# Performance work log

Hardware: AMD Instinct MI355X
Metric: run time of the kernel (lower is better)

## Reference

```python
import jax, jax.numpy as jnp
import numpy as np

N_NODES = 100000
N_EDGES = 1600000
DIM_IN, DIM_HID, DIM_OUT = 64, 128, 40


def setup_inputs() -> dict:
    key = jax.random.key(0)
    ks = jax.random.split(key, 6)
    x = jax.random.normal(ks[0], (N_NODES, DIM_IN), dtype=jnp.float32)
    edge_index = jax.random.randint(ks[1], (2, N_EDGES), 0, N_NODES, dtype=jnp.int64)
    s_in = 1.0 / np.sqrt(DIM_IN)
    s_hid = 1.0 / np.sqrt(DIM_HID)
    W1l = jax.random.normal(ks[2], (DIM_HID, DIM_IN), dtype=jnp.float32) * s_in
    W1r = jax.random.normal(ks[3], (DIM_HID, DIM_IN), dtype=jnp.float32) * s_in
    b1 = jnp.zeros((DIM_HID,), dtype=jnp.float32)
    W2l = jax.random.normal(ks[4], (DIM_OUT, DIM_HID), dtype=jnp.float32) * s_hid
    W2r = jax.random.normal(ks[5], (DIM_OUT, DIM_HID), dtype=jnp.float32) * s_hid
    b2 = jnp.zeros((DIM_OUT,), dtype=jnp.float32)
    return {"x": x, "edge_index": edge_index, "W1l": W1l, "b1": b1,
            "W1r": W1r, "W2l": W2l, "b2": b2, "W2r": W2r}


def _sage_conv(h, src, dst, Wl, bl, Wr, n_nodes):
    # mean aggregation of source-node features into target nodes
    msg = h[src]                                      # [E, d]
    agg = jax.ops.segment_sum(msg, dst, num_segments=n_nodes)
    cnt = jax.ops.segment_sum(jnp.ones((src.shape[0],), h.dtype), dst,
                              num_segments=n_nodes)
    agg = agg / jnp.maximum(cnt, 1.0)[:, None]        # [N, d]
    # PyG SAGEConv: lin_l(agg) + bias + lin_r(x) (root weight, no bias)
    return agg @ Wl.T + bl + h @ Wr.T


def reference(x, edge_index, W1l, b1, W1r, W2l, b2, W2r):
    src, dst = edge_index[0], edge_index[1]
    n = x.shape[0]
    h = _sage_conv(x, src, dst, W1l, b1, W1r, n)
    h = jax.nn.relu(h)
    out = _sage_conv(h, src, dst, W2l, b2, W2r, n)
    return jax.nn.log_softmax(out, axis=-1)
```

## Files before the change

kernel.cpp:

```cpp
#include <hip/hip_runtime.h>
#include <math.h>

#define NN 100000
#define DI 64
#define DH 128
#define DO 40

#define NBUCK 512
#define NPB 196
#define CAP 3712
#define CAPP 4352
#define EPB 4096
#define TPB_S 512
#define KE (EPB / TPB_S)

typedef __attribute__((ext_vector_type(8))) short bf16x8;
typedef __attribute__((ext_vector_type(4))) float f32x4;
typedef __attribute__((ext_vector_type(2))) float f32x2;

__device__ __forceinline__ unsigned short bf16r(float a) {
    unsigned u = __float_as_uint(a);
    u = (u + 0x7FFF + ((u >> 16) & 1)) >> 16;
    return (unsigned short)u;
}
__device__ __forceinline__ unsigned bf16pair(float a, float b) {
    return (unsigned)bf16r(a) | ((unsigned)bf16r(b) << 16);
}
__device__ __forceinline__ float bflo(unsigned u) { return __uint_as_float(u << 16); }
__device__ __forceinline__ float bfhi(unsigned u) { return __uint_as_float(u & 0xFFFF0000u); }

__global__ __launch_bounds__(TPB_S) void setup_scatter_kernel(
        const float* __restrict__ x, const float* __restrict__ W1l,
        const float* __restrict__ W1r, const float* __restrict__ W2l,
        const float* __restrict__ W2r,
        unsigned* __restrict__ xb, unsigned short* __restrict__ WB1,
        unsigned short* __restrict__ WB2, unsigned* __restrict__ p2,
        const int* __restrict__ src, const int* __restrict__ dst,
        int* __restrict__ bcur, int* __restrict__ eb,
        int nbe, int E, int N) {
    __shared__ int h[NBUCK];
    int t = threadIdx.x;
    if ((int)blockIdx.x < nbe) {
        if (t < NBUCK) h[t] = 0;
        __syncthreads();
        int base = blockIdx.x * EPB;
        int end = base + EPB; if (end > E) end = E;
        int dloc[KE];
#pragma unroll
        for (int k = 0; k < KE; k++) {
            int i = base + t + k * TPB_S;
            dloc[k] = (i < end) ? dst[i] : -1;
        }
#pragma unroll
        for (int k = 0; k < KE; k++)
            if (dloc[k] >= 0) atomicAdd(&h[(unsigned)dloc[k] / NPB], 1);
        __syncthreads();
        if (t < NBUCK) {
            int v = h[t];
            h[t] = v ? (atomicAdd(&bcur[t], v) + t * CAP) : 0;
        }
        __syncthreads();
#pragma unroll
        for (int k = 0; k < KE; k++) {
            int d = dloc[k];
            if (d >= 0) {
                unsigned bk = (unsigned)d / NPB;
                int local = d - (int)bk * NPB;
                int pos = atomicAdd(&h[bk], 1);
                eb[pos] = (local << 17) | src[base + t + k * TPB_S];
            }
        }
    } else {
        int idx = (blockIdx.x - nbe) * TPB_S + t;
        if (idx < (N + 1) * 32) {
            if (idx < N * 32) {
                float2 f = ((const float2*)x)[idx];
                xb[idx] = bf16pair(f.x, f.y);
            } else {
                xb[idx] = 0;
            }
        }
        if (idx < 16384) {
            int j = idx & 7, lane = (idx >> 3) & 63, ks = (idx >> 9) & 3, nt = idx >> 11;
            int k = ks * 32 + (lane >> 4) * 8 + j;
            int n = nt * 16 + (lane & 15);
            float v = (k < DI) ? W1l[n * DI + k] : W1r[n * DI + (k - DI)];
            WB1[idx] = bf16r(v);
        }
        if (idx >= 16384 && idx < 16384 + 10240) {
            int idx2 = idx - 16384;
            int j = idx2 & 7, lane = (idx2 >> 3) & 63, ks = (idx2 >> 9) & 3, nt = idx2 >> 11;
            int k = ks * 32 + (lane >> 4) * 8 + j;
            int n = nt * 16 + (lane & 15);
            float v = (n < DO) ? W2l[n * DH + k] : W2r[(n - DO) * DH + k];
            WB2[idx2] = bf16r(v);
        }
        if (idx < 10) p2[(size_t)N * 10 + idx] = 0;
    }
}

__global__ __launch_bounds__(256) void bucket_fill_kernel(const int* __restrict__ eb,
                                                          const int* __restrict__ bend,
                                                          int* __restrict__ rowptr,
                                                          int* __restrict__ cntg,
                                                          float* __restrict__ inv,
                                                          int* __restrict__ col, int N) {
    __shared__ int scnt[256];
    __shared__ int scur[256];
    __shared__ int sbase[256];
    int b = blockIdx.x, t = threadIdx.x;
    int ebeg = b * CAP, eend = ebeg + bend[b];
    scnt[t] = 0;
    __syncthreads();
    for (int i = ebeg + t; i < eend; i += 256)
        atomicAdd(&scnt[eb[i] >> 17], 1);
    __syncthreads();
    int myc = scnt[t];
    int pc = (myc + 3) & ~3;
    scnt[t] = pc;
    __syncthreads();
    for (int off = 1; off < 256; off <<= 1) {
        int tmp = (t >= off) ? scnt[t - off] : 0;
        __syncthreads();
        scnt[t] += tmp;
        __syncthreads();
    }
    int excl = scnt[t] - pc;
    int base = b * CAPP + excl;
    int node = b * NPB + t;
    if (t < NPB && node < N) {
        rowptr[node] = base;
        cntg[node] = myc;
        inv[node] = 1.0f / (float)(myc > 0 ? myc : 1);
    }
    scur[t] = base;
    sbase[t] = base;
    __syncthreads();
    for (int i = ebeg + t; i < eend; i += 256) {
        int pk = eb[i];
        int pos = atomicAdd(&scur[pk >> 17], 1);
        col[pos] = pk & 0x1FFFF;
    }
    __syncthreads();
    if (t < NPB) {
        int bs = sbase[t];
        for (int i = myc; i < pc; i++) col[bs + i] = NN;
    }
}

__global__ void agg1_kernel(const unsigned* __restrict__ xb, const int* __restrict__ rowptr,
                            const int* __restrict__ cnt, const float* __restrict__ inv,
                            const int* __restrict__ col, unsigned* __restrict__ xa, int N) {
    int n = (blockIdx.x * 256 + threadIdx.x) >> 3;
    int chunk = threadIdx.x & 7;
    if (n >= N) return;
    int beg = rowptr[n], deg = cnt[n];
    int degp = (deg + 3) & ~3;
    float a[8];
#pragma unroll
    for (int j = 0; j < 8; j++) a[j] = 0.f;
    for (int i = 0; i < degp; i += 4) {
        int s0 = col[beg + i], s1 = col[beg + i + 1];
        int s2 = col[beg + i + 2], s3 = col[beg + i + 3];
        uint4 u0 = *(const uint4*)(xb + (size_t)s0 * 32 + chunk * 4);
        uint4 u1 = *(const uint4*)(xb + (size_t)s1 * 32 + chunk * 4);
        uint4 u2 = *(const uint4*)(xb + (size_t)s2 * 32 + chunk * 4);
        uint4 u3 = *(const uint4*)(xb + (size_t)s3 * 32 + chunk * 4);
        a[0] += bflo(u0.x) + bflo(u1.x) + bflo(u2.x) + bflo(u3.x);
        a[1] += bfhi(u0.x) + bfhi(u1.x) + bfhi(u2.x) + bfhi(u3.x);
        a[2] += bflo(u0.y) + bflo(u1.y) + bflo(u2.y) + bflo(u3.y);
        a[3] += bfhi(u0.y) + bfhi(u1.y) + bfhi(u2.y) + bfhi(u3.y);
        a[4] += bflo(u0.z) + bflo(u1.z) + bflo(u2.z) + bflo(u3.z);
        a[5] += bfhi(u0.z) + bfhi(u1.z) + bfhi(u2.z) + bfhi(u3.z);
        a[6] += bflo(u0.w) + bflo(u1.w) + bflo(u2.w) + bflo(u3.w);
        a[7] += bfhi(u0.w) + bfhi(u1.w) + bfhi(u2.w) + bfhi(u3.w);
    }
    float invn = inv[n];
    uint4 o;
    o.x = bf16pair(a[0] * invn, a[1] * invn);
    o.y = bf16pair(a[2] * invn, a[3] * invn);
    o.z = bf16pair(a[4] * invn, a[5] * invn);
    o.w = bf16pair(a[6] * invn, a[7] * invn);
    *(uint4*)(xa + (size_t)n * 64 + chunk * 4) = o;
    uint4 u = *(const uint4*)(xb + (size_t)n * 32 + chunk * 4);
    *(uint4*)(xa + (size_t)n * 64 + 32 + chunk * 4) = u;
}

__global__ __launch_bounds__(256) void gemm12_kernel(const unsigned short* __restrict__ xa,
                                                     const unsigned short* __restrict__ WB1,
                                                     const float* __restrict__ b1,
                                                     const unsigned short* __restrict__ WB2,
                                                     const float* __restrict__ b2,
                                                     unsigned* __restrict__ p2,
                                                     float* __restrict__ selfp, int N) {
    __shared__ unsigned short hs[64][136];
    __shared__ float st[64][41];
    int w = threadIdx.x >> 6, lane = threadIdx.x & 63;
    int quad = lane >> 4, m = lane & 15;
    int rbase = blockIdx.x * 64 + w * 16;
    int arow = rbase + m; if (arow >= N) arow = N - 1;
    int lw = w * 16;

    f32x4 acc[8];
#pragma unroll
    for (int nt = 0; nt < 8; nt++) acc[nt] = (f32x4)(0.f);
#pragma unroll
    for (int ks = 0; ks < 4; ks++) {
        bf16x8 a = *(const bf16x8*)(xa + (size_t)arow * 128 + ks * 32 + quad * 8);
#pragma unroll
        for (int nt = 0; nt < 8; nt++) {
            bf16x8 b = *(const bf16x8*)(WB1 + ((size_t)(nt * 4 + ks) * 64 + lane) * 8);
            acc[nt] = __builtin_amdgcn_mfma_f32_16x16x32_bf16(a, b, acc[nt], 0, 0, 0);
        }
    }
#pragma unroll
    for (int nt = 0; nt < 8; nt++) {
        int colj = nt * 16 + m;
        float bj = b1[colj];
#pragma unroll
        for (int r = 0; r < 4; r++) {
            hs[lw + quad * 4 + r][colj] = bf16r(fmaxf(acc[nt][r] + bj, 0.f));
        }
    }
    __syncthreads();

    f32x4 acc2[5];
#pragma unroll
    for (int nt = 0; nt < 5; nt++) acc2[nt] = (f32x4)(0.f);
#pragma unroll
    for (int ks = 0; ks < 4; ks++) {
        bf16x8 a = *(const bf16x8*)(&hs[lw + m][ks * 32 + quad * 8]);
#pragma unroll
        for (int nt = 0; nt < 5; nt++) {
            bf16x8 b = *(const bf16x8*)(WB2 + ((size_t)(nt * 4 + ks) * 64 + lane) * 8);
            acc2[nt] = __builtin_amdgcn_mfma_f32_16x16x32_bf16(a, b, acc2[nt], 0, 0, 0);
        }
    }
#pragma unroll
    for (int nt = 0; nt < 5; nt++) {
        int colj = nt * 16 + m;
#pragma unroll
        for (int r = 0; r < 4; r++) {
            int lrow = lw + quad * 4 + r;
            int row = rbase + quad * 4 + r;
            float v = acc2[nt][r];
            if (colj < 40) {
                st[lrow][colj] = v;
            } else if (row < N) {
                selfp[(size_t)row * 40 + (colj - 40)] = v + b2[colj - 40];
            }
        }
    }
    __syncthreads();
    for (int i = threadIdx.x; i < 64 * 10; i += 256) {
        int lr = i / 10, dw = i - lr * 10;
        int grow = blockIdx.x * 64 + lr;
        if (grow < N) {
            float v0 = st[lr][dw * 4 + 0], v1 = st[lr][dw * 4 + 1];
            float v2 = st[lr][dw * 4 + 2], v3 = st[lr][dw * 4 + 3];
            unsigned u = __builtin_amdgcn_cvt_pk_fp8_f32(v0, v1, 0u, false);
            u = __builtin_amdgcn_cvt_pk_fp8_f32(v2, v3, u, true);
            p2[(size_t)grow * 10 + dw] = u;
        }
    }
}

__global__ void agg2_softmax_kernel(const unsigned* __restrict__ p2,
                                    const float* __restrict__ selfp,
                                    const int* __restrict__ rowptr,
                                    const int* __restrict__ cnt,
                                    const float* __restrict__ inv,
                                    const int* __restrict__ col,
                                    float* __restrict__ out, int N) {
    int n = (blockIdx.x * 256 + threadIdx.x) >> 3;
    int chunk = threadIdx.x & 7;
    if (n >= N) return;
    int beg = rowptr[n], deg = cnt[n];
    int degp = (deg + 3) & ~3;
    bool vc = (chunk < 5);
    float a[8];
#pragma unroll
    for (int j = 0; j < 8; j++) a[j] = 0.f;
    for (int i = 0; i < degp; i += 4) {
        int s0 = col[beg + i], s1 = col[beg + i + 1];
        int s2 = col[beg + i + 2], s3 = col[beg + i + 3];
        if (vc) {
            uint2 u0 = *(const uint2*)(p2 + (size_t)s0 * 10 + chunk * 2);
            uint2 u1 = *(const uint2*)(p2 + (size_t)s1 * 10 + chunk * 2);
            uint2 u2 = *(const uint2*)(p2 + (size_t)s2 * 10 + chunk * 2);
            uint2 u3 = *(const uint2*)(p2 + (size_t)s3 * 10 + chunk * 2);
            f32x2 d;
            d = __builtin_amdgcn_cvt_pk_f32_fp8(u0.x, false); a[0] += d.x; a[1] += d.y;
            d = __builtin_amdgcn_cvt_pk_f32_fp8(u0.x, true);  a[2] += d.x; a[3] += d.y;
            d = __builtin_amdgcn_cvt_pk_f32_fp8(u0.y, false); a[4] += d.x; a[5] += d.y;
            d = __builtin_amdgcn_cvt_pk_f32_fp8(u0.y, true);  a[6] += d.x; a[7] += d.y;
            d = __builtin_amdgcn_cvt_pk_f32_fp8(u1.x, false); a[0] += d.x; a[1] += d.y;
            d = __builtin_amdgcn_cvt_pk_f32_fp8(u1.x, true);  a[2] += d.x; a[3] += d.y;
            d = __builtin_amdgcn_cvt_pk_f32_fp8(u1.y, false); a[4] += d.x; a[5] += d.y;
            d = __builtin_amdgcn_cvt_pk_f32_fp8(u1.y, true);  a[6] += d.x; a[7] += d.y;
            d = __builtin_amdgcn_cvt_pk_f32_fp8(u2.x, false); a[0] += d.x; a[1] += d.y;
            d = __builtin_amdgcn_cvt_pk_f32_fp8(u2.x, true);  a[2] += d.x; a[3] += d.y;
            d = __builtin_amdgcn_cvt_pk_f32_fp8(u2.y, false); a[4] += d.x; a[5] += d.y;
            d = __builtin_amdgcn_cvt_pk_f32_fp8(u2.y, true);  a[6] += d.x; a[7] += d.y;
            d = __builtin_amdgcn_cvt_pk_f32_fp8(u3.x, false); a[0] += d.x; a[1] += d.y;
            d = __builtin_amdgcn_cvt_pk_f32_fp8(u3.x, true);  a[2] += d.x; a[3] += d.y;
            d = __builtin_amdgcn_cvt_pk_f32_fp8(u3.y, false); a[4] += d.x; a[5] += d.y;
            d = __builtin_amdgcn_cvt_pk_f32_fp8(u3.y, true);  a[6] += d.x; a[7] += d.y;
        }
    }
    float invn = inv[n];
    float v[8];
    if (vc) {
        float4 s0 = *(const float4*)(selfp + (size_t)n * DO + chunk * 8);
        float4 s1 = *(const float4*)(selfp + (size_t)n * DO + chunk * 8 + 4);
        v[0] = a[0] * invn + s0.x; v[1] = a[1] * invn + s0.y;
        v[2] = a[2] * invn + s0.z; v[3] = a[3] * invn + s0.w;
        v[4] = a[4] * invn + s1.x; v[5] = a[5] * invn + s1.y;
        v[6] = a[6] * invn + s1.z; v[7] = a[7] * invn + s1.w;
    } else {
#pragma unroll
        for (int j = 0; j < 8; j++) v[j] = 0.f;
    }
    float mv = -INFINITY;
    if (vc) {
#pragma unroll
        for (int j = 0; j < 8; j++) mv = fmaxf(mv, v[j]);
    }
#pragma unroll
    for (int off = 1; off <= 4; off <<= 1) mv = fmaxf(mv, __shfl_xor(mv, off, 8));
    float es = 0.f;
    if (vc) {
#pragma unroll
        for (int j = 0; j < 8; j++) es += expf(v[j] - mv);
    }
#pragma unroll
    for (int off = 1; off <= 4; off <<= 1) es += __shfl_xor(es, off, 8);
    if (vc) {
        float ls = mv + logf(es);
        float4 o0, o1;
        o0.x = v[0] - ls; o0.y = v[1] - ls; o0.z = v[2] - ls; o0.w = v[3] - ls;
        o1.x = v[4] - ls; o1.y = v[5] - ls; o1.z = v[6] - ls; o1.w = v[7] - ls;
        *(float4*)(out + (size_t)n * DO + chunk * 8) = o0;
        *(float4*)(out + (size_t)n * DO + chunk * 8 + 4) = o1;
    }
}

extern "C" void kernel_launch(void* const* d_in, const int* in_sizes, int n_in,
                              void* d_out, int out_size, void* d_ws, size_t ws_size,
                              hipStream_t stream) {
    const float* x   = (const float*)d_in[0];
    const int*  ei   = (const int*)d_in[1];
    const float* W1l = (const float*)d_in[2];
    const float* b1  = (const float*)d_in[3];
    const float* W1r = (const float*)d_in[4];
    const float* W2l = (const float*)d_in[5];
    const float* b2  = (const float*)d_in[6];
    const float* W2r = (const float*)d_in[7];
    float* out = (float*)d_out;

    const int E = in_sizes[1] / 2;
    const int N = NN;
    const int* src = ei;
    const int* dst = ei + E;
    const int nbe = (E + EPB - 1) / EPB;
    const int nsetup = ((N + 1) * 32 + TPB_S - 1) / TPB_S;

    size_t off = 0;
    auto alloc = [&](size_t nf) { size_t o = off; off += (nf + 63) & ~(size_t)63; return o; };
    size_t o_bcur   = alloc(NBUCK);
    size_t o_eb     = alloc((size_t)NBUCK * CAP);
    size_t o_col    = alloc((size_t)NBUCK * CAPP);
    size_t o_rowptr = alloc(N);
    size_t o_cnt    = alloc(N);
    size_t o_inv    = alloc(N);
    size_t o_xb     = alloc((size_t)(N + 1) * 32);
    size_t o_xa     = alloc((size_t)N * 64);
    size_t o_p2     = alloc((size_t)(N + 1) * 10);
    size_t o_selfp  = alloc((size_t)N * DO);
    size_t o_wb1    = alloc(16384 / 2);
    size_t o_wb2    = alloc(10240 / 2);
    (void)ws_size;

    float* ws = (float*)d_ws;
    int* bcur   = (int*)(ws + o_bcur);
    int* eb     = (int*)(ws + o_eb);
    int* col    = (int*)(ws + o_col);
    int* rowptr = (int*)(ws + o_rowptr);
    int* cnt    = (int*)(ws + o_cnt);
    float* inv  = ws + o_inv;
    unsigned* xb = (unsigned*)(ws + o_xb);
    unsigned* xa = (unsigned*)(ws + o_xa);
    unsigned* p2 = (unsigned*)(ws + o_p2);
    float* selfp = ws + o_selfp;
    unsigned short* WB1 = (unsigned short*)(ws + o_wb1);
    unsigned short* WB2 = (unsigned short*)(ws + o_wb2);

    hipMemsetAsync(bcur, 0, NBUCK * sizeof(int), stream);

    setup_scatter_kernel<<<nbe + nsetup, TPB_S, 0, stream>>>(
        x, W1l, W1r, W2l, W2r, xb, WB1, WB2, p2, src, dst, bcur, eb, nbe, E, N);

    bucket_fill_kernel<<<NBUCK, 256, 0, stream>>>(eb, bcur, rowptr, cnt, inv, col, N);

    agg1_kernel<<<(N * 8 + 255) / 256, 256, 0, stream>>>(xb, rowptr, cnt, inv, col, xa, N);
    gemm12_kernel<<<(N + 63) / 64, 256, 0, stream>>>((const unsigned short*)xa, WB1, b1,
                                                     WB2, b2, p2, selfp, N);
    agg2_softmax_kernel<<<(N * 8 + 255) / 256, 256, 0, stream>>>(p2, selfp, rowptr, cnt, inv, col, out, N);
}
```

Before: 203.4 us.

## Fuse layer-1 neighbor aggregation into the GEMM kernel via shared memory

The first-layer mean aggregation and the two fused GEMMs now run in one kernel. Each block gathers and averages neighbor features for its 64 nodes into shared memory and then feeds them directly to the MFMA stage. This removes the xa intermediate buffer's global write and read and one kernel launch. In exchange each block runs the gather with 2 iterations of 32 nodes per thread-group, and the gemm grid has fewer blocks than agg1 had, which may reduce latency hiding for the irregular gather.

```diff
diff --git a/kernel.cpp b/kernel.cpp
--- a/kernel.cpp
+++ b/kernel.cpp
@@ -148,57 +148,62 @@
     }
 }
 
-__global__ void agg1_kernel(const unsigned* __restrict__ xb, const int* __restrict__ rowptr,
-                            const int* __restrict__ cnt, const float* __restrict__ inv,
-                            const int* __restrict__ col, unsigned* __restrict__ xa, int N) {
-    int n = (blockIdx.x * 256 + threadIdx.x) >> 3;
-    int chunk = threadIdx.x & 7;
-    if (n >= N) return;
-    int beg = rowptr[n], deg = cnt[n];
-    int degp = (deg + 3) & ~3;
-    float a[8];
-#pragma unroll
-    for (int j = 0; j < 8; j++) a[j] = 0.f;
-    for (int i = 0; i < degp; i += 4) {
-        int s0 = col[beg + i], s1 = col[beg + i + 1];
-        int s2 = col[beg + i + 2], s3 = col[beg + i + 3];
-        uint4 u0 = *(const uint4*)(xb + (size_t)s0 * 32 + chunk * 4);
-        uint4 u1 = *(const uint4*)(xb + (size_t)s1 * 32 + chunk * 4);
-        uint4 u2 = *(const uint4*)(xb + (size_t)s2 * 32 + chunk * 4);
-        uint4 u3 = *(const uint4*)(xb + (size_t)s3 * 32 + chunk * 4);
-        a[0] += bflo(u0.x) + bflo(u1.x) + bflo(u2.x) + bflo(u3.x);
-        a[1] += bfhi(u0.x) + bfhi(u1.x) + bfhi(u2.x) + bfhi(u3.x);
-        a[2] += bflo(u0.y) + bflo(u1.y) + bflo(u2.y) + bflo(u3.y);
-        a[3] += bfhi(u0.y) + bfhi(u1.y) + bfhi(u2.y) + bfhi(u3.y);
-        a[4] += bflo(u0.z) + bflo(u1.z) + bflo(u2.z) + bflo(u3.z);
-        a[5] += bfhi(u0.z) + bfhi(u1.z) + bfhi(u2.z) + bfhi(u3.z);
-        a[6] += bflo(u0.w) + bflo(u1.w) + bflo(u2.w) + bflo(u3.w);
-        a[7] += bfhi(u0.w) + bfhi(u1.w) + bfhi(u2.w) + bfhi(u3.w);
-    }
-    float invn = inv[n];
-    uint4 o;
-    o.x = bf16pair(a[0] * invn, a[1] * invn);
-    o.y = bf16pair(a[2] * invn, a[3] * invn);
-    o.z = bf16pair(a[4] * invn, a[5] * invn);
-    o.w = bf16pair(a[6] * invn, a[7] * invn);
-    *(uint4*)(xa + (size_t)n * 64 + chunk * 4) = o;
-    uint4 u = *(const uint4*)(xb + (size_t)n * 32 + chunk * 4);
-    *(uint4*)(xa + (size_t)n * 64 + 32 + chunk * 4) = u;
-}
-
-__global__ __launch_bounds__(256) void gemm12_kernel(const unsigned short* __restrict__ xa,
-                                                     const unsigned short* __restrict__ WB1,
-                                                     const float* __restrict__ b1,
-                                                     const unsigned short* __restrict__ WB2,
-                                                     const float* __restrict__ b2,
-                                                     unsigned* __restrict__ p2,
-                                                     float* __restrict__ selfp, int N) {
-    __shared__ unsigned short hs[64][136];
+__global__ __launch_bounds__(256) void agg_gemm12_kernel(
+        const unsigned* __restrict__ xb, const int* __restrict__ rowptr,
+        const int* __restrict__ cnt, const float* __restrict__ inv,
+        const int* __restrict__ col,
+        const unsigned short* __restrict__ WB1, const float* __restrict__ b1,
+        const unsigned short* __restrict__ WB2, const float* __restrict__ b2,
+        unsigned* __restrict__ p2, float* __restrict__ selfp, int N) {
+    __shared__ unsigned short sh[64][136];
     __shared__ float st[64][41];
-    int w = threadIdx.x >> 6, lane = threadIdx.x & 63;
+    int t = threadIdx.x;
+    int g = t >> 3, chunk = t & 7;
+
+#pragma unroll
+    for (int it = 0; it < 2; ++it) {
+        int lr = it * 32 + g;
+        int n = blockIdx.x * 64 + lr;
+        float a[8];
+#pragma unroll
+        for (int j = 0; j < 8; j++) a[j] = 0.f;
+        float invn = 0.f;
+        uint4 u = make_uint4(0, 0, 0, 0);
+        if (n < N) {
+            int beg = rowptr[n], deg = cnt[n];
+            int degp = (deg + 3) & ~3;
+            for (int i = 0; i < degp; i += 4) {
+                int s0 = col[beg + i], s1 = col[beg + i + 1];
+                int s2 = col[beg + i + 2], s3 = col[beg + i + 3];
+                uint4 u0 = *(const uint4*)(xb + (size_t)s0 * 32 + chunk * 4);
+                uint4 u1 = *(const uint4*)(xb + (size_t)s1 * 32 + chunk * 4);
+                uint4 u2 = *(const uint4*)(xb + (size_t)s2 * 32 + chunk * 4);
+                uint4 u3 = *(const uint4*)(xb + (size_t)s3 * 32 + chunk * 4);
+                a[0] += bflo(u0.x) + bflo(u1.x) + bflo(u2.x) + bflo(u3.x);
+                a[1] += bfhi(u0.x) + bfhi(u1.x) + bfhi(u2.x) + bfhi(u3.x);
+                a[2] += bflo(u0.y) + bflo(u1.y) + bflo(u2.y) + bflo(u3.y);
+                a[3] += bfhi(u0.y) + bfhi(u1.y) + bfhi(u2.y) + bfhi(u3.y);
+                a[4] += bflo(u0.z) + bflo(u1.z) + bflo(u2.z) + bflo(u3.z);
+                a[5] += bfhi(u0.z) + bfhi(u1.z) + bfhi(u2.z) + bfhi(u3.z);
+                a[6] += bflo(u0.w) + bflo(u1.w) + bflo(u2.w) + bflo(u3.w);
+                a[7] += bfhi(u0.w) + bfhi(u1.w) + bfhi(u2.w) + bfhi(u3.w);
+            }
+            invn = inv[n];
+            u = *(const uint4*)(xb + (size_t)n * 32 + chunk * 4);
+        }
+        uint4 o;
+        o.x = bf16pair(a[0] * invn, a[1] * invn);
+        o.y = bf16pair(a[2] * invn, a[3] * invn);
+        o.z = bf16pair(a[4] * invn, a[5] * invn);
+        o.w = bf16pair(a[6] * invn, a[7] * invn);
+        *(uint4*)&sh[lr][chunk * 8] = o;
+        *(uint4*)&sh[lr][64 + chunk * 8] = u;
+    }
+    __syncthreads();
+
+    int w = t >> 6, lane = t & 63;
     int quad = lane >> 4, m = lane & 15;
     int rbase = blockIdx.x * 64 + w * 16;
-    int arow = rbase + m; if (arow >= N) arow = N - 1;
     int lw = w * 16;
 
     f32x4 acc[8];
@@ -206,20 +211,21 @@
     for (int nt = 0; nt < 8; nt++) acc[nt] = (f32x4)(0.f);
 #pragma unroll
     for (int ks = 0; ks < 4; ks++) {
-        bf16x8 a = *(const bf16x8*)(xa + (size_t)arow * 128 + ks * 32 + quad * 8);
+        bf16x8 a = *(const bf16x8*)(&sh[lw + m][ks * 32 + quad * 8]);
 #pragma unroll
         for (int nt = 0; nt < 8; nt++) {
             bf16x8 b = *(const bf16x8*)(WB1 + ((size_t)(nt * 4 + ks) * 64 + lane) * 8);
             acc[nt] = __builtin_amdgcn_mfma_f32_16x16x32_bf16(a, b, acc[nt], 0, 0, 0);
         }
     }
+    __syncthreads();
 #pragma unroll
     for (int nt = 0; nt < 8; nt++) {
         int colj = nt * 16 + m;
         float bj = b1[colj];
 #pragma unroll
         for (int r = 0; r < 4; r++) {
-            hs[lw + quad * 4 + r][colj] = bf16r(fmaxf(acc[nt][r] + bj, 0.f));
+            sh[lw + quad * 4 + r][colj] = bf16r(fmaxf(acc[nt][r] + bj, 0.f));
         }
     }
     __syncthreads();
@@ -229,7 +235,7 @@
     for (int nt = 0; nt < 5; nt++) acc2[nt] = (f32x4)(0.f);
 #pragma unroll
     for (int ks = 0; ks < 4; ks++) {
-        bf16x8 a = *(const bf16x8*)(&hs[lw + m][ks * 32 + quad * 8]);
+        bf16x8 a = *(const bf16x8*)(&sh[lw + m][ks * 32 + quad * 8]);
 #pragma unroll
         for (int nt = 0; nt < 5; nt++) {
             bf16x8 b = *(const bf16x8*)(WB2 + ((size_t)(nt * 4 + ks) * 64 + lane) * 8);
@@ -252,7 +258,7 @@
         }
     }
     __syncthreads();
-    for (int i = threadIdx.x; i < 64 * 10; i += 256) {
+    for (int i = t; i < 64 * 10; i += 256) {
         int lr = i / 10, dw = i - lr * 10;
         int grow = blockIdx.x * 64 + lr;
         if (grow < N) {
@@ -374,7 +380,6 @@
     size_t o_cnt    = alloc(N);
     size_t o_inv    = alloc(N);
     size_t o_xb     = alloc((size_t)(N + 1) * 32);
-    size_t o_xa     = alloc((size_t)N * 64);
     size_t o_p2     = alloc((size_t)(N + 1) * 10);
     size_t o_selfp  = alloc((size_t)N * DO);
     size_t o_wb1    = alloc(16384 / 2);
@@ -389,7 +394,6 @@
     int* cnt    = (int*)(ws + o_cnt);
     float* inv  = ws + o_inv;
     unsigned* xb = (unsigned*)(ws + o_xb);
-    unsigned* xa = (unsigned*)(ws + o_xa);
     unsigned* p2 = (unsigned*)(ws + o_p2);
     float* selfp = ws + o_selfp;
     unsigned short* WB1 = (unsigned short*)(ws + o_wb1);
@@ -402,8 +406,8 @@
 
     bucket_fill_kernel<<<NBUCK, 256, 0, stream>>>(eb, bcur, rowptr, cnt, inv, col, N);
 
-    agg1_kernel<<<(N * 8 + 255) / 256, 256, 0, stream>>>(xb, rowptr, cnt, inv, col, xa, N);
-    gemm12_kernel<<<(N + 63) / 64, 256, 0, stream>>>((const unsigned short*)xa, WB1, b1,
-                                                     WB2, b2, p2, selfp, N);
+    agg_gemm12_kernel<<<(N + 63) / 64, 256, 0, stream>>>(
+        xb, rowptr, cnt, inv, col, WB1, b1, WB2, b2, p2, selfp, N);
+
     agg2_softmax_kernel<<<(N * 8 + 255) / 256, 256, 0, stream>>>(p2, selfp, rowptr, cnt, inv, col, out, N);
 }
```

Measured after the change: 199.6 us. No clear change (-1.9%).
